# Kernel optimization log

Measured on AMD Instinct MI355X. Metric: run time of the kernel, lower is better.

The kernel has to match this reference:

```python
import jax, jax.numpy as jnp
import numpy as np

B, DIN, H, DOUT = 4096, 2048, 4096, 2048


def setup_inputs() -> dict:
    key = jax.random.key(0)
    ks = jax.random.split(key, 17)
    x = jax.random.normal(ks[0], (B, DIN), dtype=jnp.float32)
    W0 = jax.random.randint(ks[1], (H, DIN), -127, 128, dtype=jnp.int32)
    b0 = jax.random.randint(ks[2], (H,), -127, 128, dtype=jnp.int32)
    W2 = jax.random.randint(ks[3], (H, H), -127, 128, dtype=jnp.int32)
    b2 = jax.random.randint(ks[4], (H,), -127, 128, dtype=jnp.int32)
    W4 = jax.random.randint(ks[5], (DOUT, H), -127, 128, dtype=jnp.int32)
    b4 = jax.random.randint(ks[6], (DOUT,), -127, 128, dtype=jnp.int32)
    # amax scalars: positive calibration ranges in [0.5, 2.0)
    amaxes = [jax.random.uniform(ks[7 + i], (), jnp.float32, 0.5, 2.0) for i in range(9)]
    (a0_in, a0_w, a0_b, a2_in, a2_w, a2_b, a4_in, a4_w, a4_b) = amaxes
    return {"x": x, "W0": W0, "b0": b0, "W2": W2, "b2": b2, "W4": W4, "b4": b4,
            "a0_in": a0_in, "a0_w": a0_w, "a0_b": a0_b,
            "a2_in": a2_in, "a2_w": a2_w, "a2_b": a2_b,
            "a4_in": a4_in, "a4_w": a4_w, "a4_b": a4_b}


def _quant(x, amax):
    # torch: clamp(round(x * 127/amax), -127, 127).int()
    scale = 127.0 / amax
    return jnp.clip(jnp.round(x * scale), -127.0, 127.0).astype(jnp.int32)


def _layer(x, W, b, a_in, a_w, a_b):
    xq = _quant(x, a_in)                                      # [B, in] int32
    acc = jnp.matmul(xq, W.T, preferred_element_type=jnp.int32)  # [B, out] int32
    y = acc.astype(jnp.float32) * (a_w * a_in / (127.0 ** 2))    # double dequant
    return y + b.astype(jnp.float32) * (a_b / 127.0)             # single dequant bias


def reference(x, W0, b0, W2, b2, W4, b4,
              a0_in, a0_w, a0_b, a2_in, a2_w, a2_b, a4_in, a4_w, a4_b):
    x = x.reshape(x.shape[0], -1)
    x = _layer(x, W0, b0, a0_in, a0_w, a0_b)
    x = jax.nn.relu(x)
    x = _layer(x, W2, b2, a2_in, a2_w, a2_b)
    x = jax.nn.relu(x)
    x = _layer(x, W4, b4, a4_in, a4_w, a4_b)
    return x
```

## Files before the change

kernel.cpp:

```cpp
#include <hip/hip_runtime.h>

using i32x4 = __attribute__((ext_vector_type(4))) int;

#define DEVI static __device__ __forceinline__

DEVI void gload_lds16(const void* g, void* l) {
  __builtin_amdgcn_global_load_lds(
      (const __attribute__((address_space(1))) void*)g,
      (__attribute__((address_space(3))) void*)l, 16, 0, 0);
}

template <int N> DEVI void vmcnt_n() {
  asm volatile("s_waitcnt vmcnt(%0)" ::"n"(N) : "memory");
}
template <int N> DEVI void lgkm_n() {
  asm volatile("s_waitcnt lgkmcnt(%0)" ::"n"(N) : "memory");
}

#define FENCE() asm volatile("" ::: "memory")
#define BARX()                    \
  do {                            \
    FENCE();                      \
    __builtin_amdgcn_s_barrier(); \
    FENCE();                      \
  } while (0)
#define SCHB() __builtin_amdgcn_sched_barrier(0)
#define PRIO1() __builtin_amdgcn_s_setprio(1)
#define PRIO0() __builtin_amdgcn_s_setprio(0)

__global__ void __launch_bounds__(256) pack_w_kernel(const int* __restrict__ w,
                                                     signed char* __restrict__ o,
                                                     int n4) {
  int stride = gridDim.x * blockDim.x;
  for (int i = blockIdx.x * blockDim.x + threadIdx.x; i < n4; i += stride) {
    int4 v = reinterpret_cast<const int4*>(w)[i];
    char4 c;
    c.x = (signed char)v.x;
    c.y = (signed char)v.y;
    c.z = (signed char)v.z;
    c.w = (signed char)v.w;
    reinterpret_cast<char4*>(o)[i] = c;
  }
}

__global__ void __launch_bounds__(256) quant_x_kernel(const float* __restrict__ x,
                                                      signed char* __restrict__ o,
                                                      const float* __restrict__ amax,
                                                      int n4) {
  const float s = 127.0f / amax[0];
  int stride = gridDim.x * blockDim.x;
  for (int i = blockIdx.x * blockDim.x + threadIdx.x; i < n4; i += stride) {
    float4 v = reinterpret_cast<const float4*>(x)[i];
    char4 c;
    float q;
    q = fminf(fmaxf(rintf(__fmul_rn(v.x, s)), -127.0f), 127.0f); c.x = (signed char)(int)q;
    q = fminf(fmaxf(rintf(__fmul_rn(v.y, s)), -127.0f), 127.0f); c.y = (signed char)(int)q;
    q = fminf(fmaxf(rintf(__fmul_rn(v.z, s)), -127.0f), 127.0f); c.z = (signed char)(int)q;
    q = fminf(fmaxf(rintf(__fmul_rn(v.w, s)), -127.0f), 127.0f); c.w = (signed char)(int)q;
    reinterpret_cast<char4*>(o)[i] = c;
  }
}


#define GB(b, j, k0_)                                           \
  gload_lds16(Wb + (size_t)((j)*64 + srow) * K + (k0_),         \
              &lds[b][ABYTES + (j)*8192 + tid * 16])
#define GA(b, r0, k0_)                                          \
  gload_lds16(Ab + (size_t)((r0) + srow) * K + (k0_),           \
              &lds[b][(r0)*128 + tid * 16])

#define STG_B_EARLY(b, kt)                                              \
  do {                                                                  \
    const int k0_ = (kt)*128 + scol;                                    \
    _Pragma("unroll") for (int j = 0; j < NBE; ++j) GB(b, j, k0_);      \
  } while (0)
#define STG_B_LATE(b, kt)                                               \
  do {                                                                  \
    const int k0_ = (kt)*128 + scol;                                    \
    _Pragma("unroll") for (int j = NBE; j < NN; ++j) GB(b, j, k0_);     \
  } while (0)
#define STG_A01(b, kt)               \
  do {                               \
    const int k0_ = (kt)*128 + scol; \
    GA(b, 0, k0_);                   \
    GA(b, 128, k0_);                 \
  } while (0)
#define STG_A23(b, kt)               \
  do {                               \
    const int k0_ = (kt)*128 + scol; \
    GA(b, 64, k0_);                  \
    GA(b, 192, k0_);                 \
  } while (0)

#define AF_(b, m, h) \
  (*(const i32x4*)&lds[b][(wrl + (m)*16 + ro) * 128 + ((h) ? cS1 : cS0)])
#define BF_(b, n, h) \
  (*(const i32x4*)&lds[b][ABYTES + (wcl + (n)*16 + ro) * 128 + ((h) ? cS1 : cS0)])

#define RD_AF(dst, b, m0)            \
  do {                               \
    dst[0][0] = AF_(b, m0, 0);       \
    dst[0][1] = AF_(b, m0, 1);       \
    dst[1][0] = AF_(b, (m0) + 1, 0); \
    dst[1][1] = AF_(b, (m0) + 1, 1); \
  } while (0)

#define READ_BF(b)                                   \
  do {                                               \
    _Pragma("unroll") for (int n = 0; n < NN; ++n) { \
      bf[n][0] = BF_(b, n, 0);                       \
      bf[n][1] = BF_(b, n, 1);                       \
    }                                                \
  } while (0)

#define MFMA_P(mp, af)                                                                     \
  do {                                                                                     \
    _Pragma("unroll") for (int n = 0; n < NN; ++n) {                                       \
      acc[2 * (mp)][n] =                                                                   \
          __builtin_amdgcn_mfma_i32_16x16x64_i8(af[0][0], bf[n][0], acc[2 * (mp)][n], 0, 0, 0); \
      acc[2 * (mp)][n] =                                                                   \
          __builtin_amdgcn_mfma_i32_16x16x64_i8(af[0][1], bf[n][1], acc[2 * (mp)][n], 0, 0, 0); \
      acc[2 * (mp) + 1][n] = __builtin_amdgcn_mfma_i32_16x16x64_i8(                        \
          af[1][0], bf[n][0], acc[2 * (mp) + 1][n], 0, 0, 0);                              \
      acc[2 * (mp) + 1][n] = __builtin_amdgcn_mfma_i32_16x16x64_i8(                        \
          af[1][1], bf[n][1], acc[2 * (mp) + 1][n], 0, 0, 0);                              \
    }                                                                                      \
  } while (0)

#define TILE_STEADY(b, t)                       \
  do {                                          \
    READ_BF(b);                                 \
    RD_AF(afB, b, 2);                           \
    STG_B_LATE(1 - (b), (t) + 1);               \
    STG_A01(1 - (b), (t) + 1);                  \
    vmcnt_n<NN + 2>();                          \
    BARX(); lgkm_n<4>(); SCHB();                \
    PRIO1(); MFMA_P(0, afA); PRIO0();           \
    RD_AF(afA, b, 4);                           \
    STG_A23(1 - (b), (t) + 1);                  \
    BARX(); lgkm_n<4>(); SCHB();                \
    PRIO1(); MFMA_P(1, afB); PRIO0();           \
    RD_AF(afB, b, 6);                           \
    vmcnt_n<2>();                               \
    BARX(); lgkm_n<4>(); SCHB();                \
    PRIO1(); MFMA_P(2, afA); PRIO0();           \
    RD_AF(afA, 1 - (b), 0);                     \
    if ((t) + 2 < nt) STG_B_EARLY(b, (t) + 2);  \
    BARX(); lgkm_n<4>(); SCHB();                \
    PRIO1(); MFMA_P(3, afB); PRIO0();           \
  } while (0)

#define TILE_LAST(b)                            \
  do {                                          \
    READ_BF(b);                                 \
    RD_AF(afB, b, 2);                           \
    vmcnt_n<0>();                               \
    BARX(); lgkm_n<4>(); SCHB();                \
    PRIO1(); MFMA_P(0, afA); PRIO0();           \
    RD_AF(afA, b, 4);                           \
    BARX(); lgkm_n<4>(); SCHB();                \
    PRIO1(); MFMA_P(1, afB); PRIO0();           \
    RD_AF(afB, b, 6);                           \
    BARX(); lgkm_n<4>(); SCHB();                \
    PRIO1(); MFMA_P(2, afA); PRIO0();           \
    BARX(); lgkm_n<0>(); SCHB();                \
    PRIO1(); MFMA_P(3, afB); PRIO0();           \
  } while (0)

template <int BN, int OUT_I8>
__global__ __launch_bounds__(512, 2) void gemm8_kernel(
    const signed char* __restrict__ A, const signed char* __restrict__ W,
    const int* __restrict__ bias, void* __restrict__ out, int M, int N, int K,
    const float* __restrict__ p_ain, const float* __restrict__ p_aw,
    const float* __restrict__ p_ab, const float* __restrict__ p_anext) {
  static_assert(BN == 256 || BN == 128, "");
  constexpr int NN = BN / 64;
  constexpr int NBE = NN / 2;
  constexpr int ABYTES = 256 * 128;
  __shared__ signed char lds[2][ABYTES + BN * 128];

  const int tid = threadIdx.x;
  const int lane = tid & 63;
  const int wave = tid >> 6;
  const int wrl = (wave >> 2) * 128;
  const int wcl = (wave & 3) * (BN / 4);
  const int tileM = blockIdx.y * 256;
  const int tileN = blockIdx.x * BN;

  const signed char* Ab = A + (size_t)tileM * K;
  const signed char* Wb = W + (size_t)tileN * K;

  const int srow = tid >> 3;
  const int scol = ((tid & 7) ^ (srow & 7)) * 16;

  const int ro = lane & 15;
  const int kg = lane >> 4;
  const int cS0 = ((kg ^ (ro & 7)) << 4);
  const int cS1 = (((4 + kg) ^ (ro & 7)) << 4);

  const int nt = K >> 7;

  i32x4 acc[8][NN] = {};
  i32x4 afA[2][2], afB[2][2], bf[NN][2];

  {
    const int k0_ = scol;
#pragma unroll
    for (int j = 0; j < NN; ++j) GB(0, j, k0_);
    GA(0, 0, k0_);
    GA(0, 128, k0_);
    GA(0, 64, k0_);
    GA(0, 192, k0_);
  }
  FENCE();
  STG_B_EARLY(1, 1);
  vmcnt_n<NBE>();
  BARX();
  RD_AF(afA, 0, 0);

  for (int t = 0; t < nt - 2; t += 2) {
    TILE_STEADY(0, t);
    TILE_STEADY(1, t + 1);
  }
  TILE_STEADY(0, nt - 2);
  TILE_LAST(1);

  const float s1 = __fmul_rn(p_aw[0], p_ain[0]) / 16129.0f;
  const float s2 = p_ab[0] / 127.0f;
  float qs = 0.0f;
  if (OUT_I8) qs = 127.0f / p_anext[0];

#pragma unroll
  for (int m = 0; m < 8; ++m) {
#pragma unroll
    for (int n = 0; n < NN; ++n) {
      const int col = tileN + wcl + n * 16 + ro;
      const int row0 = tileM + wrl + m * 16 + kg * 4;
      const float bv = __fmul_rn((float)bias[col], s2);
#pragma unroll
      for (int i = 0; i < 4; ++i) {
        float y = __fadd_rn(__fmul_rn((float)acc[m][n][i], s1), bv);
        if (OUT_I8) {
          float rl = fmaxf(y, 0.0f);
          float q = fminf(rintf(__fmul_rn(rl, qs)), 127.0f);
          ((signed char*)out)[(size_t)(row0 + i) * N + col] = (signed char)(int)q;
        } else {
          ((float*)out)[(size_t)(row0 + i) * N + col] = y;
        }
      }
    }
  }
}

extern "C" void kernel_launch(void* const* d_in, const int* in_sizes, int n_in,
                              void* d_out, int out_size, void* d_ws, size_t ws_size,
                              hipStream_t stream) {
  const float* x = (const float*)d_in[0];
  const int* W0 = (const int*)d_in[1];
  const int* b0 = (const int*)d_in[2];
  const int* W2 = (const int*)d_in[3];
  const int* b2 = (const int*)d_in[4];
  const int* W4 = (const int*)d_in[5];
  const int* b4 = (const int*)d_in[6];
  const float* a0_in = (const float*)d_in[7];
  const float* a0_w = (const float*)d_in[8];
  const float* a0_b = (const float*)d_in[9];
  const float* a2_in = (const float*)d_in[10];
  const float* a2_w = (const float*)d_in[11];
  const float* a2_b = (const float*)d_in[12];
  const float* a4_in = (const float*)d_in[13];
  const float* a4_w = (const float*)d_in[14];
  const float* a4_b = (const float*)d_in[15];

  constexpr int Bb = 4096, DIN = 2048, H = 4096, DOUT = 2048;
  constexpr size_t MB = 1u << 20;

  char* ws = (char*)d_ws;
  signed char* xq0 = (signed char*)(ws);
  signed char* xq2 = (signed char*)(ws);
  signed char* W0q = (signed char*)(ws + 8 * MB);
  signed char* W2q = (signed char*)(ws + 16 * MB);
  signed char* W4q = (signed char*)(ws + 32 * MB);
  signed char* xq1 = (signed char*)(ws + 40 * MB);

  pack_w_kernel<<<2048, 256, 0, stream>>>(W0, W0q, H * DIN / 4);
  pack_w_kernel<<<2048, 256, 0, stream>>>(W2, W2q, H * H / 4);
  pack_w_kernel<<<2048, 256, 0, stream>>>(W4, W4q, DOUT * H / 4);
  quant_x_kernel<<<2048, 256, 0, stream>>>(x, xq0, a0_in, Bb * DIN / 4);

  gemm8_kernel<256, 1><<<dim3(H / 256, Bb / 256), 512, 0, stream>>>(
      xq0, W0q, b0, xq1, Bb, H, DIN, a0_in, a0_w, a0_b, a2_in);
  gemm8_kernel<256, 1><<<dim3(H / 256, Bb / 256), 512, 0, stream>>>(
      xq1, W2q, b2, xq2, Bb, H, H, a2_in, a2_w, a2_b, a4_in);
  gemm8_kernel<128, 0><<<dim3(DOUT / 128, Bb / 256), 512, 0, stream>>>(
      xq2, W4q, b4, d_out, Bb, DOUT, H, a4_in, a4_w, a4_b, a4_in);
}
```

Baseline: 166.4 us.

## Switch int8 GEMM from 16x16x64 to 32x32x32 MFMA tiles

Replaces the 16x16x64 int8 MFMA instruction with the 32x32x32 variant. LDS fragment reads are regrouped into 32-row slices with a matching XOR swizzle, and the accumulators become 16-wide vectors. The epilogue row and column mapping is rewritten for the 32x32 output layout. The larger MFMA tile should cut LDS fragment reads per FLOP and may raise MFMA throughput, but the writes it produces are more scattered per lane and register pressure may go up.

New measurement: 189.1 us. +13.7%, slower.

```diff
diff --git a/kernel.cpp b/kernel.cpp
--- a/kernel.cpp
+++ b/kernel.cpp
@@ -1,6 +1,7 @@
 #include <hip/hip_runtime.h>
 
 using i32x4 = __attribute__((ext_vector_type(4))) int;
+using i32x16 = __attribute__((ext_vector_type(16))) int;
 
 #define DEVI static __device__ __forceinline__
 
@@ -92,83 +93,78 @@
     GA(b, 192, k0_);                 \
   } while (0)
 
-#define AF_(b, m, h) \
-  (*(const i32x4*)&lds[b][(wrl + (m)*16 + ro) * 128 + ((h) ? cS1 : cS0)])
-#define BF_(b, n, h) \
-  (*(const i32x4*)&lds[b][ABYTES + (wcl + (n)*16 + ro) * 128 + ((h) ? cS1 : cS0)])
-
-#define RD_AF(dst, b, m0)            \
-  do {                               \
-    dst[0][0] = AF_(b, m0, 0);       \
-    dst[0][1] = AF_(b, m0, 1);       \
-    dst[1][0] = AF_(b, (m0) + 1, 0); \
-    dst[1][1] = AF_(b, (m0) + 1, 1); \
-  } while (0)
-
-#define READ_BF(b)                                   \
-  do {                                               \
-    _Pragma("unroll") for (int n = 0; n < NN; ++n) { \
-      bf[n][0] = BF_(b, n, 0);                       \
-      bf[n][1] = BF_(b, n, 1);                       \
-    }                                                \
-  } while (0)
-
-#define MFMA_P(mp, af)                                                                     \
-  do {                                                                                     \
-    _Pragma("unroll") for (int n = 0; n < NN; ++n) {                                       \
-      acc[2 * (mp)][n] =                                                                   \
-          __builtin_amdgcn_mfma_i32_16x16x64_i8(af[0][0], bf[n][0], acc[2 * (mp)][n], 0, 0, 0); \
-      acc[2 * (mp)][n] =                                                                   \
-          __builtin_amdgcn_mfma_i32_16x16x64_i8(af[0][1], bf[n][1], acc[2 * (mp)][n], 0, 0, 0); \
-      acc[2 * (mp) + 1][n] = __builtin_amdgcn_mfma_i32_16x16x64_i8(                        \
-          af[1][0], bf[n][0], acc[2 * (mp) + 1][n], 0, 0, 0);                              \
-      acc[2 * (mp) + 1][n] = __builtin_amdgcn_mfma_i32_16x16x64_i8(                        \
-          af[1][1], bf[n][1], acc[2 * (mp) + 1][n], 0, 0, 0);                              \
-    }                                                                                      \
+#define RD_AF32(dst, b, mi)                                                 \
+  do {                                                                      \
+    const int ab_ = (wrl + (mi)*32 + ro32) * 128;                           \
+    dst[0] = *(const i32x4*)&lds[b][ab_ + sl0];                             \
+    dst[1] = *(const i32x4*)&lds[b][ab_ + sl1];                             \
+    dst[2] = *(const i32x4*)&lds[b][ab_ + sl2];                             \
+    dst[3] = *(const i32x4*)&lds[b][ab_ + sl3];                             \
+  } while (0)
+
+#define READ_BF32(b)                                                        \
+  do {                                                                      \
+    _Pragma("unroll") for (int n = 0; n < NW; ++n) {                        \
+      const int bb_ = ABYTES + (wcl + n * 32 + ro32) * 128;                 \
+      bf[n][0] = *(const i32x4*)&lds[b][bb_ + sl0];                         \
+      bf[n][1] = *(const i32x4*)&lds[b][bb_ + sl1];                         \
+      bf[n][2] = *(const i32x4*)&lds[b][bb_ + sl2];                         \
+      bf[n][3] = *(const i32x4*)&lds[b][bb_ + sl3];                         \
+    }                                                                       \
+  } while (0)
+
+#define MFMA_W(mi, af)                                                      \
+  do {                                                                      \
+    _Pragma("unroll") for (int kh = 0; kh < 4; ++kh) {                      \
+      _Pragma("unroll") for (int n = 0; n < NW; ++n) {                      \
+        acc[mi][n] = __builtin_amdgcn_mfma_i32_32x32x32_i8(                 \
+            af[kh], bf[n][kh], acc[mi][n], 0, 0, 0);                        \
+      }                                                                     \
+    }                                                                       \
   } while (0)
 
 #define TILE_STEADY(b, t)                       \
   do {                                          \
-    READ_BF(b);                                 \
-    RD_AF(afB, b, 2);                           \
+    READ_BF32(b);                               \
+    RD_AF32(afB, b, 1);                         \
     STG_B_LATE(1 - (b), (t) + 1);               \
     STG_A01(1 - (b), (t) + 1);                  \
     vmcnt_n<NN + 2>();                          \
     BARX(); lgkm_n<4>(); SCHB();                \
-    PRIO1(); MFMA_P(0, afA); PRIO0();           \
-    RD_AF(afA, b, 4);                           \
+    PRIO1(); MFMA_W(0, afA); PRIO0();           \
+    RD_AF32(afA, b, 2);                         \
     STG_A23(1 - (b), (t) + 1);                  \
     BARX(); lgkm_n<4>(); SCHB();                \
-    PRIO1(); MFMA_P(1, afB); PRIO0();           \
-    RD_AF(afB, b, 6);                           \
+    PRIO1(); MFMA_W(1, afB); PRIO0();           \
+    RD_AF32(afB, b, 3);                         \
     vmcnt_n<2>();                               \
     BARX(); lgkm_n<4>(); SCHB();                \
-    PRIO1(); MFMA_P(2, afA); PRIO0();           \
-    RD_AF(afA, 1 - (b), 0);                     \
+    PRIO1(); MFMA_W(2, afA); PRIO0();           \
+    RD_AF32(afA, 1 - (b), 0);                   \
     if ((t) + 2 < nt) STG_B_EARLY(b, (t) + 2);  \
     BARX(); lgkm_n<4>(); SCHB();                \
-    PRIO1(); MFMA_P(3, afB); PRIO0();           \
+    PRIO1(); MFMA_W(3, afB); PRIO0();           \
   } while (0)
 
 #define TILE_LAST(b)                            \
   do {                                          \
-    READ_BF(b);                                 \
-    RD_AF(afB, b, 2);                           \
+    READ_BF32(b);                               \
+    RD_AF32(afB, b, 1);                         \
     vmcnt_n<0>();                               \
     BARX(); lgkm_n<4>(); SCHB();                \
-    PRIO1(); MFMA_P(0, afA); PRIO0();           \
-    RD_AF(afA, b, 4);                           \
-    BARX(); lgkm_n<4>(); SCHB();                \
-    PRIO1(); MFMA_P(1, afB); PRIO0();           \
-    RD_AF(afB, b, 6);                           \
-    BARX(); lgkm_n<4>(); SCHB();                \
-    PRIO1(); MFMA_P(2, afA); PRIO0();           \
+    PRIO1(); MFMA_W(0, afA); PRIO0();           \
+    RD_AF32(afA, b, 2);                         \
+    BARX(); lgkm_n<4>(); SCHB();                \
+    PRIO1(); MFMA_W(1, afB); PRIO0();           \
+    RD_AF32(afB, b, 3);                         \
+    BARX(); lgkm_n<4>(); SCHB();                \
+    PRIO1(); MFMA_W(2, afA); PRIO0();           \
     BARX(); lgkm_n<0>(); SCHB();                \
-    PRIO1(); MFMA_P(3, afB); PRIO0();           \
+    PRIO1(); MFMA_W(3, afB); PRIO0();           \
   } while (0)
 
 template <int BN, int OUT_I8>
-__global__ __launch_bounds__(512, 2) void gemm8_kernel(
+__global__ __launch_bounds__(512, 2) void gemm32_kernel(
     const signed char* __restrict__ A, const signed char* __restrict__ W,
     const int* __restrict__ bias, void* __restrict__ out, int M, int N, int K,
     const float* __restrict__ p_ain, const float* __restrict__ p_aw,
@@ -176,6 +172,7 @@
   static_assert(BN == 256 || BN == 128, "");
   constexpr int NN = BN / 64;
   constexpr int NBE = NN / 2;
+  constexpr int NW = BN / 128;
   constexpr int ABYTES = 256 * 128;
   __shared__ signed char lds[2][ABYTES + BN * 128];
 
@@ -193,15 +190,18 @@
   const int srow = tid >> 3;
   const int scol = ((tid & 7) ^ (srow & 7)) * 16;
 
-  const int ro = lane & 15;
-  const int kg = lane >> 4;
-  const int cS0 = ((kg ^ (ro & 7)) << 4);
-  const int cS1 = (((4 + kg) ^ (ro & 7)) << 4);
+  const int ro32 = lane & 31;
+  const int hv = lane >> 5;
+  const int lx = lane & 7;
+  const int sl0 = ((0 * 2 + hv) ^ lx) << 4;
+  const int sl1 = ((1 * 2 + hv) ^ lx) << 4;
+  const int sl2 = ((2 * 2 + hv) ^ lx) << 4;
+  const int sl3 = ((3 * 2 + hv) ^ lx) << 4;
 
   const int nt = K >> 7;
 
-  i32x4 acc[8][NN] = {};
-  i32x4 afA[2][2], afB[2][2], bf[NN][2];
+  i32x16 acc[4][NW] = {};
+  i32x4 afA[4], afB[4], bf[NW][4];
 
   {
     const int k0_ = scol;
@@ -216,7 +216,7 @@
   STG_B_EARLY(1, 1);
   vmcnt_n<NBE>();
   BARX();
-  RD_AF(afA, 0, 0);
+  RD_AF32(afA, 0, 0);
 
   for (int t = 0; t < nt - 2; t += 2) {
     TILE_STEADY(0, t);
@@ -231,21 +231,21 @@
   if (OUT_I8) qs = 127.0f / p_anext[0];
 
 #pragma unroll
-  for (int m = 0; m < 8; ++m) {
-#pragma unroll
-    for (int n = 0; n < NN; ++n) {
-      const int col = tileN + wcl + n * 16 + ro;
-      const int row0 = tileM + wrl + m * 16 + kg * 4;
+  for (int mi = 0; mi < 4; ++mi) {
+#pragma unroll
+    for (int n = 0; n < NW; ++n) {
+      const int col = tileN + wcl + n * 32 + ro32;
       const float bv = __fmul_rn((float)bias[col], s2);
 #pragma unroll
-      for (int i = 0; i < 4; ++i) {
-        float y = __fadd_rn(__fmul_rn((float)acc[m][n][i], s1), bv);
+      for (int r = 0; r < 16; ++r) {
+        const int row = tileM + wrl + mi * 32 + (r & 3) + 8 * (r >> 2) + 4 * hv;
+        float y = __fadd_rn(__fmul_rn((float)acc[mi][n][r], s1), bv);
         if (OUT_I8) {
           float rl = fmaxf(y, 0.0f);
           float q = fminf(rintf(__fmul_rn(rl, qs)), 127.0f);
-          ((signed char*)out)[(size_t)(row0 + i) * N + col] = (signed char)(int)q;
+          ((signed char*)out)[(size_t)row * N + col] = (signed char)(int)q;
         } else {
-          ((float*)out)[(size_t)(row0 + i) * N + col] = y;
+          ((float*)out)[(size_t)row * N + col] = y;
         }
       }
     }
@@ -288,10 +288,10 @@
   pack_w_kernel<<<2048, 256, 0, stream>>>(W4, W4q, DOUT * H / 4);
   quant_x_kernel<<<2048, 256, 0, stream>>>(x, xq0, a0_in, Bb * DIN / 4);
 
-  gemm8_kernel<256, 1><<<dim3(H / 256, Bb / 256), 512, 0, stream>>>(
+  gemm32_kernel<256, 1><<<dim3(H / 256, Bb / 256), 512, 0, stream>>>(
       xq0, W0q, b0, xq1, Bb, H, DIN, a0_in, a0_w, a0_b, a2_in);
-  gemm8_kernel<256, 1><<<dim3(H / 256, Bb / 256), 512, 0, stream>>>(
+  gemm32_kernel<256, 1><<<dim3(H / 256, Bb / 256), 512, 0, stream>>>(
       xq1, W2q, b2, xq2, Bb, H, H, a2_in, a2_w, a2_b, a4_in);
-  gemm8_kernel<128, 0><<<dim3(DOUT / 128, Bb / 256), 512, 0, stream>>>(
+  gemm32_kernel<128, 0><<<dim3(DOUT / 128, Bb / 256), 512, 0, stream>>>(
       xq2, W4q, b4, d_out, Bb, DOUT, H, a4_in, a4_w, a4_b, a4_in);
 }
```
